# Kernel tuning notes

Measured on AMD Instinct MI355X. Metric: run time of the kernel, lower is better.

Reference implementation:

```python
import jax, jax.numpy as jnp
import numpy as np
from jax import lax

B, T, D = 1, 2048, 2048
H, KVH, HD = 16, 4, 128
BETA = 0.9
ROPE_BASE = 10000.0


def _causal_prefix_ema(x, beta):
    # x: (B, T, D); m_t = beta * m_{t-1} + (1 - beta) * x_t, m_{-1} = 0
    def step(m, xt):
        m = beta * m + (1.0 - beta) * xt
        return m, m
    _, ys = lax.scan(step, jnp.zeros_like(x[:, 0]), jnp.swapaxes(x, 0, 1))
    return jnp.swapaxes(ys, 0, 1)


def _rotate_half(x):
    x1, x2 = jnp.split(x, 2, axis=-1)
    return jnp.concatenate([-x2, x1], axis=-1)


def _rope_cos_sin(t, hd, dtype):
    inv_freq = 1.0 / (ROPE_BASE ** (jnp.arange(0, hd, 2, dtype=jnp.float32) / hd))
    freqs = jnp.arange(t, dtype=jnp.float32)[:, None] * inv_freq[None, :]  # (T, HD/2)
    emb = jnp.concatenate([freqs, freqs], axis=-1)  # (T, HD)
    return jnp.cos(emb).astype(dtype)[None, None], jnp.sin(emb).astype(dtype)[None, None]


def setup_inputs() -> dict:
    key = jax.random.key(0)
    ks = jax.random.split(key, 8)
    std = 0.02
    return {
        "hidden_states": jax.random.normal(ks[0], (B, T, D), jnp.float32),
        "Wq": jax.random.normal(ks[1], (D, H * HD), jnp.float32) * std,
        "Wk": jax.random.normal(ks[2], (D, KVH * HD), jnp.float32) * std,
        "Wv": jax.random.normal(ks[3], (D, KVH * HD), jnp.float32) * std,
        "Wo": jax.random.normal(ks[4], (H * HD, D), jnp.float32) * std,
        "Wr1": jax.random.normal(ks[5], (D, D // 2), jnp.float32) * std,
        "br1": jnp.zeros((D // 2,), jnp.float32),
        "Wr2": jax.random.normal(ks[6], (D // 2, 2), jnp.float32) * std,
        "br2": jnp.zeros((2,), jnp.float32),
    }


def reference(hidden_states, Wq, Wk, Wv, Wo, Wr1, br1, Wr2, br2):
    b, t, d = hidden_states.shape
    q = hidden_states @ Wq  # (B, T, H*HD)

    # multi-level memories: l1 = raw, l2 = causal prefix EMA
    l2 = _causal_prefix_ema(hidden_states, BETA)

    # router MLP on q + softmax over levels
    h = jax.nn.silu(q @ Wr1 + br1)
    lam = jax.nn.softmax(h @ Wr2 + br2, axis=-1)  # (B, T, 2)
    fused = lam[..., 0:1] * hidden_states + lam[..., 1:2] * l2

    # shape to heads
    q_s = q.reshape(b, t, H, HD).transpose(0, 2, 1, 3)                 # (B, H, T, HD)
    k_s = (fused @ Wk).reshape(b, t, KVH, HD).transpose(0, 2, 1, 3)    # (B, KVH, T, HD)
    v_s = (fused @ Wv).reshape(b, t, KVH, HD).transpose(0, 2, 1, 3)

    # RoPE
    cos, sin = _rope_cos_sin(t, HD, q_s.dtype)
    q_s = q_s * cos + _rotate_half(q_s) * sin
    k_s = k_s * cos + _rotate_half(k_s) * sin

    # repeat kv for GQA
    n_rep = H // KVH
    k_s = jnp.repeat(k_s, n_rep, axis=1)
    v_s = jnp.repeat(v_s, n_rep, axis=1)

    # causal SDPA
    scale = 1.0 / jnp.sqrt(jnp.asarray(HD, q_s.dtype))
    scores = jnp.einsum("bhqd,bhkd->bhqk", q_s, k_s) * scale
    causal = jnp.tril(jnp.ones((t, t), dtype=bool))
    scores = jnp.where(causal[None, None], scores, jnp.finfo(scores.dtype).min)
    attn = jax.nn.softmax(scores, axis=-1)
    out = jnp.einsum("bhqk,bhkd->bhqd", attn, v_s)  # (B, H, T, HD)

    out = out.transpose(0, 2, 1, 3).reshape(b, t, H * HD)
    return out @ Wo
```

## Files before the change

kernel.cpp:

```cpp
#include <hip/hip_runtime.h>
#include <hip/hip_bf16.h>

#define T_SEQ 2048
#define D_MODEL 2048
#define NH 16
#define NKVH 4
#define HD 128

typedef __attribute__((ext_vector_type(8))) short bf16x8;
typedef __attribute__((ext_vector_type(4))) float f32x4;

static __device__ __forceinline__ short f32_to_bf16(float f) {
    unsigned u = __float_as_uint(f);
    u += 0x7fffu + ((u >> 16) & 1u);
    return (short)(u >> 16);
}
static __device__ __forceinline__ float bf16_to_f32(short s) {
    return __uint_as_float(((unsigned)(unsigned short)s) << 16);
}
static __device__ __forceinline__ void gl_to_lds16(const void* g, void* l) {
    __builtin_amdgcn_global_load_lds(
        (const __attribute__((address_space(1))) unsigned int*)g,
        (__attribute__((address_space(3))) unsigned int*)l, 16, 0, 0);
}

template<int BN>
__global__ __launch_bounds__(256, 2) void gemm_bt_kernel(
    const short* __restrict__ A, const short* __restrict__ Bt,
    float* __restrict__ Cf, short* __restrict__ Cb,
    int M, int N, int K, const float* __restrict__ bias, int act)
{
    constexpr int NI = BN / 64;
    constexpr int BCH = BN / 32;
    __shared__ short Alds[3][64 * 64];
    __shared__ short Blds[3][BN * 64];

    const int tid = threadIdx.x;
    const int wave = tid >> 6, lane = tid & 63;
    const int l16 = lane & 15, quad = lane >> 4;
    const int wn = wave * (BN / 4);
    const int m0 = blockIdx.y * 64, n0 = blockIdx.x * BN;
    const int niter = K >> 6;

    f32x4 acc[4][NI] = {};

    #pragma unroll
    for (int st = 0; st < 2; ++st) {
        int kk0 = st << 6;
        #pragma unroll
        for (int p = 0; p < 2; ++p) {
            int li = p * 256 + tid;
            int row = li >> 3, sc = li & 7;
            gl_to_lds16(A + (size_t)(m0 + row) * K + kk0 + ((sc ^ (row & 7)) * 8),
                        &Alds[st][(size_t)(p * 256 + wave * 64) * 8]);
        }
        #pragma unroll
        for (int p = 0; p < BCH; ++p) {
            int li = p * 256 + tid;
            int row = li >> 3, sc = li & 7;
            gl_to_lds16(Bt + (size_t)(n0 + row) * K + kk0 + ((sc ^ (row & 7)) * 8),
                        &Blds[st][(size_t)(p * 256 + wave * 64) * 8]);
        }
    }

    int cur = 0, stg = 2;
    for (int t = 0; t < niter; ++t) {
        if (t + 1 < niter) {
            if constexpr (BN == 128)
                asm volatile("s_waitcnt vmcnt(6)\n\ts_barrier" ::: "memory");
            else
                asm volatile("s_waitcnt vmcnt(4)\n\ts_barrier" ::: "memory");
        } else {
            asm volatile("s_waitcnt vmcnt(0)\n\ts_barrier" ::: "memory");
        }

        if (t + 2 < niter) {
            int k1 = (t + 2) << 6;
            #pragma unroll
            for (int p = 0; p < 2; ++p) {
                int li = p * 256 + tid;
                int row = li >> 3, sc = li & 7;
                gl_to_lds16(A + (size_t)(m0 + row) * K + k1 + ((sc ^ (row & 7)) * 8),
                            &Alds[stg][(size_t)(p * 256 + wave * 64) * 8]);
            }
            #pragma unroll
            for (int p = 0; p < BCH; ++p) {
                int li = p * 256 + tid;
                int row = li >> 3, sc = li & 7;
                gl_to_lds16(Bt + (size_t)(n0 + row) * K + k1 + ((sc ^ (row & 7)) * 8),
                            &Blds[stg][(size_t)(p * 256 + wave * 64) * 8]);
            }
        }

        const short* Ab = Alds[cur];
        const short* Bb = Blds[cur];
        #pragma unroll
        for (int kk = 0; kk < 2; ++kk) {
            bf16x8 a[4], b[NI];
            #pragma unroll
            for (int i = 0; i < 4; ++i)
                a[i] = *(const bf16x8*)
                    &Ab[(size_t)(i * 16 + l16) * 64 + (((kk * 4 + quad) ^ (l16 & 7)) * 8)];
            #pragma unroll
            for (int i = 0; i < NI; ++i)
                b[i] = *(const bf16x8*)
                    &Bb[(size_t)(wn + i * 16 + l16) * 64 + (((kk * 4 + quad) ^ (l16 & 7)) * 8)];
            #pragma unroll
            for (int mi = 0; mi < 4; ++mi)
                #pragma unroll
                for (int ni = 0; ni < NI; ++ni)
                    acc[mi][ni] = __builtin_amdgcn_mfma_f32_16x16x32_bf16(
                        a[mi], b[ni], acc[mi][ni], 0, 0, 0);
        }
        cur = (cur == 2) ? 0 : cur + 1;
        stg = (stg == 2) ? 0 : stg + 1;
    }

    #pragma unroll
    for (int mi = 0; mi < 4; ++mi) {
        #pragma unroll
        for (int ni = 0; ni < NI; ++ni) {
            int col = n0 + wn + ni * 16 + l16;
            float bv = bias ? bias[col] : 0.0f;
            #pragma unroll
            for (int r = 0; r < 4; ++r) {
                int row = m0 + mi * 16 + quad * 4 + r;
                float x = acc[mi][ni][r] + bv;
                if (act) x = x / (1.0f + __expf(-x));
                size_t o = (size_t)row * N + col;
                if (Cf) Cf[o] = x;
                if (Cb) Cb[o] = f32_to_bf16(x);
            }
        }
    }
}

__global__ __launch_bounds__(256) void transpose_all_kernel(
    const float* __restrict__ Wq, const float* __restrict__ Wk,
    const float* __restrict__ Wv, const float* __restrict__ Wr1,
    const float* __restrict__ Wo, short* __restrict__ Wq_t,
    short* __restrict__ Wkv_t, short* __restrict__ Wr1_t,
    short* __restrict__ Wo_t)
{
    __shared__ float tile[32][33];
    int bx = blockIdx.x;
    const float* src; short* dst; int ld, cb;
    if (bx < 64)       { src = Wq;  dst = Wq_t;  ld = 2048; cb = bx; }
    else if (bx < 80)  { src = Wk;  dst = Wkv_t; ld = 512;  cb = bx - 64; }
    else if (bx < 96)  { src = Wv;  dst = Wkv_t + (size_t)512 * 2048; ld = 512; cb = bx - 80; }
    else if (bx < 128) { src = Wr1; dst = Wr1_t; ld = 1024; cb = bx - 96; }
    else               { src = Wo;  dst = Wo_t;  ld = 2048; cb = bx - 128; }
    int c0 = cb * 32, r0 = blockIdx.y * 32;
    int t = threadIdx.x;
    int r = t >> 3, c4 = (t & 7) * 4;
    float4 v = *(const float4*)&src[(size_t)(r0 + r) * ld + c0 + c4];
    tile[r][c4 + 0] = v.x; tile[r][c4 + 1] = v.y;
    tile[r][c4 + 2] = v.z; tile[r][c4 + 3] = v.w;
    __syncthreads();
    short o[4];
    #pragma unroll
    for (int j = 0; j < 4; ++j) o[j] = f32_to_bf16(tile[c4 + j][r]);
    *(uint2*)&dst[(size_t)(c0 + r) * 2048 + r0 + c4] = *(const uint2*)o;
}

__global__ __launch_bounds__(256) void transpose_bf_kernel(
    const short* __restrict__ src, int ld, short* __restrict__ dst, int ldd)
{
    __shared__ float tile[32][33];
    int r0 = blockIdx.y * 32, c0 = blockIdx.x * 32;
    int x = threadIdx.x & 31, y = threadIdx.x >> 5;
    #pragma unroll
    for (int i = 0; i < 4; ++i)
        tile[y + i * 8][x] = bf16_to_f32(src[(size_t)(r0 + y + i * 8) * ld + c0 + x]);
    __syncthreads();
    #pragma unroll
    for (int i = 0; i < 4; ++i)
        dst[(size_t)(c0 + y + i * 8) * ldd + r0 + x] = f32_to_bf16(tile[x][y + i * 8]);
}

__global__ __launch_bounds__(256) void ema_kernel(const float* __restrict__ hs,
                                                  float* __restrict__ l2,
                                                  short* __restrict__ hs_b)
{
    int d = blockIdx.y * 256 + threadIdx.x;
    int t0 = blockIdx.x * 128;
    int ts = t0 - 192; if (ts < 0) ts = 0;
    float m = 0.0f;
    for (int tb = ts; tb < t0; tb += 16) {
        float buf[16];
        #pragma unroll
        for (int j = 0; j < 16; ++j) buf[j] = hs[(size_t)(tb + j) * D_MODEL + d];
        #pragma unroll
        for (int j = 0; j < 16; ++j) m = 0.9f * m + 0.1f * buf[j];
    }
    for (int tb = t0; tb < t0 + 128; tb += 16) {
        float buf[16];
        #pragma unroll
        for (int j = 0; j < 16; ++j) buf[j] = hs[(size_t)(tb + j) * D_MODEL + d];
        #pragma unroll
        for (int j = 0; j < 16; ++j) hs_b[(size_t)(tb + j) * D_MODEL + d] = f32_to_bf16(buf[j]);
        #pragma unroll
        for (int j = 0; j < 16; ++j) { m = 0.9f * m + 0.1f * buf[j]; buf[j] = m; }
        #pragma unroll
        for (int j = 0; j < 16; ++j) l2[(size_t)(tb + j) * D_MODEL + d] = buf[j];
    }
}

__global__ __launch_bounds__(64) void lam_kernel(
    const short* __restrict__ h, const float* __restrict__ Wr2,
    const float* __restrict__ br2, float* __restrict__ lam)
{
    int t = blockIdx.x;
    int lane = threadIdx.x;
    float z0 = 0.0f, z1 = 0.0f;
    for (int i = lane; i < 1024; i += 64) {
        float hv = bf16_to_f32(h[(size_t)t * 1024 + i]);
        z0 += hv * Wr2[i * 2 + 0];
        z1 += hv * Wr2[i * 2 + 1];
    }
    #pragma unroll
    for (int off = 1; off < 64; off <<= 1) {
        z0 += __shfl_xor(z0, off);
        z1 += __shfl_xor(z1, off);
    }
    if (lane == 0) {
        z0 += br2[0]; z1 += br2[1];
        float mx = fmaxf(z0, z1);
        float e0 = expf(z0 - mx), e1 = expf(z1 - mx);
        float inv = 1.0f / (e0 + e1);
        lam[t * 2 + 0] = e0 * inv;
        lam[t * 2 + 1] = e1 * inv;
    }
}

__global__ void fuse_kernel(const float* __restrict__ hs, const float* __restrict__ l2,
                            const float* __restrict__ lam, short* __restrict__ fused)
{
    int idx = blockIdx.x * blockDim.x + threadIdx.x;
    int t = idx >> 9;
    float a0 = lam[t * 2 + 0], a1 = lam[t * 2 + 1];
    float4 a = ((const float4*)hs)[idx];
    float4 b = ((const float4*)l2)[idx];
    short o[4] = {f32_to_bf16(a0 * a.x + a1 * b.x), f32_to_bf16(a0 * a.y + a1 * b.y),
                  f32_to_bf16(a0 * a.z + a1 * b.z), f32_to_bf16(a0 * a.w + a1 * b.w)};
    *(uint2*)(fused + (size_t)idx * 4) = *(const uint2*)o;
}

__global__ void rope_q_kernel(const short* __restrict__ q, short* __restrict__ qr)
{
    int idx = blockIdx.x * blockDim.x + threadIdx.x;
    int d = idx & 63;
    int h = (idx >> 6) & 15;
    int t = idx >> 10;
    float fr = (float)t * __expf(-(float)d * 0.14391156831212787f);
    float s, c;
    sincosf(fr, &s, &c);
    const float sc = 0.08838834764831845f;
    const short* src = q + (size_t)t * D_MODEL + h * HD;
    float x1 = bf16_to_f32(src[d]) * sc, x2 = bf16_to_f32(src[d + 64]) * sc;
    short* dst = qr + ((size_t)h * T_SEQ + t) * HD;
    dst[d]      = f32_to_bf16(x1 * c - x2 * s);
    dst[d + 64] = f32_to_bf16(x2 * c + x1 * s);
}

__global__ void rope_k_kernel(const short* __restrict__ kv, short* __restrict__ kr)
{
    int idx = blockIdx.x * blockDim.x + threadIdx.x;
    int d = idx & 63;
    int kh = (idx >> 6) & 3;
    int t = idx >> 8;
    float fr = (float)t * __expf(-(float)d * 0.14391156831212787f);
    float s, c;
    sincosf(fr, &s, &c);
    const short* src = kv + (size_t)t * 1024 + kh * HD;
    float x1 = bf16_to_f32(src[d]), x2 = bf16_to_f32(src[d + 64]);
    short* dst = kr + ((size_t)kh * T_SEQ + t) * HD;
    dst[d]      = f32_to_bf16(x1 * c - x2 * s);
    dst[d + 64] = f32_to_bf16(x2 * c + x1 * s);
}

__global__ __launch_bounds__(512, 2) void attn_kernel(
    const short* __restrict__ Qr, const short* __restrict__ Kr,
    const short* __restrict__ Vt, short* __restrict__ Out)
{
    const int h = blockIdx.x;
    const int y = blockIdx.y;
    const int kvh = h >> 2;
    const int tid = threadIdx.x;
    const int wave = tid >> 6, lane = tid & 63;
    const int l16 = lane & 15, quad = lane >> 4;
    const int wq = wave & 1;
    const int wk = wave >> 1;

    __shared__ __align__(16) char smem[147456];
    short* Klds = (short*)smem;
    short* Vlds = (short*)(smem + 65536);
    short* Plds = (short*)(smem + 131072);

    const short* kbase = Kr + (size_t)kvh * T_SEQ * HD;
    const short* vbase = Vt + (size_t)kvh * HD * T_SEQ;

    #pragma unroll 1
    for (int ph = 0; ph < 2; ++ph) {
        const int qt32 = ph ? (31 - y) : y;
        const int qbase = qt32 * 64 + wq * 32;
        const int n = (qt32 >> 1) + 1;
        const int ko = wk * 32;

        bf16x8 qf[2][4];
        #pragma unroll
        for (int m = 0; m < 2; ++m) {
            const short* qrow = Qr + ((size_t)h * T_SEQ + qbase + m * 16 + l16) * HD;
            #pragma unroll
            for (int kc = 0; kc < 4; ++kc)
                qf[m][kc] = *(const bf16x8*)&qrow[kc * 32 + quad * 8];
        }
        f32x4 o[2][8] = {};
        float lsum[2][4] = {};

        __syncthreads();

        {
            #pragma unroll
            for (int p = 0; p < 4; ++p) {
                int li = p * 512 + tid;
                int row = li >> 4, gs = (li & 15) ^ (row & 15);
                gl_to_lds16(kbase + (size_t)row * HD + gs * 8,
                            &Klds[(size_t)(p * 512 + wave * 64) * 8]);
            }
            #pragma unroll
            for (int p = 0; p < 4; ++p) {
                int li = p * 512 + tid;
                int row = li >> 4, gs = (li & 15) ^ (row & 15);
                gl_to_lds16(vbase + (size_t)row * T_SEQ + gs * 8,
                            &Vlds[(size_t)(p * 512 + wave * 64) * 8]);
            }
        }

        for (int t = 0; t < n; ++t) {
            asm volatile("s_waitcnt vmcnt(0)\n\ts_barrier" ::: "memory");

            if (t + 1 < n) {
                int kv1 = (t + 1) << 7;
                int nb = (t + 1) & 1;
                const short* ks = kbase + (size_t)kv1 * HD;
                #pragma unroll
                for (int p = 0; p < 4; ++p) {
                    int li = p * 512 + tid;
                    int row = li >> 4, gs = (li & 15) ^ (row & 15);
                    gl_to_lds16(ks + (size_t)row * HD + gs * 8,
                                &Klds[(size_t)(nb * 16384 + (p * 512 + wave * 64) * 8)]);
                }
                #pragma unroll
                for (int p = 0; p < 4; ++p) {
                    int li = p * 512 + tid;
                    int row = li >> 4, gs = (li & 15) ^ (row & 15);
                    gl_to_lds16(vbase + (size_t)row * T_SEQ + kv1 + gs * 8,
                                &Vlds[(size_t)(nb * 16384 + (p * 512 + wave * 64) * 8)]);
                }
            }

            const short* Kb = Klds + (size_t)(t & 1) * 16384;
            const short* Vb = Vlds + (size_t)(t & 1) * 16384;

            f32x4 s[2][2];
            #pragma unroll
            for (int m = 0; m < 2; ++m)
                #pragma unroll
                for (int ni = 0; ni < 2; ++ni) s[m][ni] = (f32x4){0, 0, 0, 0};
            __builtin_amdgcn_s_setprio(1);
            #pragma unroll
            for (int ni = 0; ni < 2; ++ni)
                #pragma unroll
                for (int kc = 0; kc < 4; ++kc) {
                    bf16x8 b = *(const bf16x8*)
                        &Kb[(size_t)(ko + ni * 16 + l16) * 128 + (((kc * 4 + quad) ^ l16) * 8)];
                    s[0][ni] = __builtin_amdgcn_mfma_f32_16x16x32_bf16(qf[0][kc], b, s[0][ni], 0, 0, 0);
                    s[1][ni] = __builtin_amdgcn_mfma_f32_16x16x32_bf16(qf[1][kc], b, s[1][ni], 0, 0, 0);
                }
            __builtin_amdgcn_s_setprio(0);

            if (t == n - 1) {
                int kvg0 = (t << 7) + ko;
                #pragma unroll
                for (int m = 0; m < 2; ++m)
                    #pragma unroll
                    for (int ni = 0; ni < 2; ++ni) {
                        int kvg = kvg0 + ni * 16 + l16;
                        #pragma unroll
                        for (int r = 0; r < 4; ++r) {
                            int qg = qbase + m * 16 + quad * 4 + r;
                            float p = (kvg <= qg) ? __expf(s[m][ni][r]) : 0.0f;
                            lsum[m][r] += p;
                            int prow = quad * 4 + r, pcol = ni * 16 + l16;
                            int slot = (pcol >> 3) ^ (prow & 3) ^ quad;
                            Plds[wave * 1024 + (m * 16 + prow) * 32 +
                                 slot * 8 + (pcol & 7)] = f32_to_bf16(p);
                        }
                    }
            } else {
                #pragma unroll
                for (int m = 0; m < 2; ++m)
                    #pragma unroll
                    for (int ni = 0; ni < 2; ++ni)
                        #pragma unroll
                        for (int r = 0; r < 4; ++r) {
                            float p = __expf(s[m][ni][r]);
                            lsum[m][r] += p;
                            int prow = quad * 4 + r, pcol = ni * 16 + l16;
                            int slot = (pcol >> 3) ^ (prow & 3) ^ quad;
                            Plds[wave * 1024 + (m * 16 + prow) * 32 +
                                 slot * 8 + (pcol & 7)] = f32_to_bf16(p);
                        }
            }
            asm volatile("s_waitcnt lgkmcnt(0)" ::: "memory");

            __builtin_amdgcn_s_setprio(1);
            {
                int slot0 = quad ^ (l16 & 3) ^ ((l16 >> 2) & 3);
                bf16x8 pa0 = *(const bf16x8*)
                    &Plds[wave * 1024 + l16 * 32 + slot0 * 8];
                bf16x8 pa1 = *(const bf16x8*)
                    &Plds[wave * 1024 + (16 + l16) * 32 + slot0 * 8];
                #pragma unroll
                for (int d8 = 0; d8 < 8; ++d8) {
                    bf16x8 b = *(const bf16x8*)
                        &Vb[(size_t)(d8 * 16 + l16) * 128 +
                            (((wk * 4 + quad) ^ l16) * 8)];
                    o[0][d8] = __builtin_amdgcn_mfma_f32_16x16x32_bf16(pa0, b, o[0][d8], 0, 0, 0);
                    o[1][d8] = __builtin_amdgcn_mfma_f32_16x16x32_bf16(pa1, b, o[1][d8], 0, 0, 0);
                }
            }
            __builtin_amdgcn_s_setprio(0);
        }

        __syncthreads();
        float* Ox = (float*)smem;
        float* Lx = (float*)(smem + 101376);
        if (wk) {
            int base = (wq * 3 + wk - 1) * 32;
            #pragma unroll
            for (int m = 0; m < 2; ++m)
                #pragma unroll
                for (int d8 = 0; d8 < 8; ++d8)
                    #pragma unroll
                    for (int r = 0; r < 4; ++r)
                        Ox[(base + m * 16 + quad * 4 + r) * 132 + d8 * 16 + l16] = o[m][d8][r];
            #pragma unroll
            for (int m = 0; m < 2; ++m)
                #pragma unroll
                for (int r = 0; r < 4; ++r)
                    Lx[(base + m * 16 + quad * 4 + r) * 16 + l16] = lsum[m][r];
        }
        __syncthreads();
        if (wk == 0) {
            #pragma unroll
            for (int j = 0; j < 3; ++j)
                #pragma unroll
                for (int m = 0; m < 2; ++m)
                    #pragma unroll
                    for (int d8 = 0; d8 < 8; ++d8)
                        #pragma unroll
                        for (int r = 0; r < 4; ++r)
                            o[m][d8][r] += Ox[((wq * 3 + j) * 32 + m * 16 + quad * 4 + r) * 132
                                              + d8 * 16 + l16];
            #pragma unroll
            for (int m = 0; m < 2; ++m)
                #pragma unroll
                for (int r = 0; r < 4; ++r) {
                    #pragma unroll
                    for (int j = 0; j < 3; ++j)
                        lsum[m][r] += Lx[((wq * 3 + j) * 32 + m * 16 + quad * 4 + r) * 16 + l16];
                    #pragma unroll
                    for (int off = 1; off < 16; off <<= 1)
                        lsum[m][r] += __shfl_xor(lsum[m][r], off);
                    lsum[m][r] = 1.0f / lsum[m][r];
                }
            #pragma unroll
            for (int m = 0; m < 2; ++m)
                #pragma unroll
                for (int d8 = 0; d8 < 8; ++d8)
                    #pragma unroll
                    for (int r = 0; r < 4; ++r) {
                        int row = qbase + m * 16 + quad * 4 + r;
                        Out[(size_t)row * D_MODEL + h * HD + d8 * 16 + l16] =
                            f32_to_bf16(o[m][d8][r] * lsum[m][r]);
                    }
        }
    }
}

extern "C" void kernel_launch(void* const* d_in, const int* in_sizes, int n_in,
                              void* d_out, int out_size, void* d_ws, size_t ws_size,
                              hipStream_t stream)
{
    const float* hs  = (const float*)d_in[0];
    const float* Wq  = (const float*)d_in[1];
    const float* Wk  = (const float*)d_in[2];
    const float* Wv  = (const float*)d_in[3];
    const float* Wo  = (const float*)d_in[4];
    const float* Wr1 = (const float*)d_in[5];
    const float* br1 = (const float*)d_in[6];
    const float* Wr2 = (const float*)d_in[7];
    const float* br2 = (const float*)d_in[8];
    float* out = (float*)d_out;

    char* w = (char*)d_ws;
    const size_t MB = 1u << 20;
    float* l2_f     = (float*)(w + 0 * MB);
    short* hs_bf    = (short*)(w + 16 * MB);
    short* Wq_t     = (short*)(w + 24 * MB);
    short* Wkv_t    = (short*)(w + 32 * MB);
    short* Wr1_t    = (short*)(w + 36 * MB);
    short* Wo_t     = (short*)(w + 40 * MB);
    short* q_bf     = (short*)(w + 48 * MB);
    short* h_bf     = (short*)(w + 56 * MB);
    short* fused_bf = (short*)(w + 60 * MB);
    short* kv_bf    = (short*)(w + 68 * MB);
    short* qr       = (short*)(w + 72 * MB);
    short* kr       = (short*)(w + 80 * MB);
    short* vr       = (short*)(w + 82 * MB);
    float* lam_f    = (float*)(w + 84 * MB);
    short* attn_bf  = hs_bf;

    transpose_all_kernel<<<dim3(192, 64), 256, 0, stream>>>(
        Wq, Wk, Wv, Wr1, Wo, Wq_t, Wkv_t, Wr1_t, Wo_t);

    ema_kernel<<<dim3(T_SEQ / 128, D_MODEL / 256), 256, 0, stream>>>(hs, l2_f, hs_bf);

    gemm_bt_kernel<128><<<dim3(16, 32), 256, 0, stream>>>(
        hs_bf, Wq_t, nullptr, q_bf, 2048, 2048, 2048, nullptr, 0);

    gemm_bt_kernel<64><<<dim3(16, 32), 256, 0, stream>>>(
        q_bf, Wr1_t, nullptr, h_bf, 2048, 1024, 2048, br1, 1);

    lam_kernel<<<T_SEQ, 64, 0, stream>>>(h_bf, Wr2, br2, lam_f);

    fuse_kernel<<<(T_SEQ * D_MODEL / 4) / 256, 256, 0, stream>>>(hs, l2_f, lam_f, fused_bf);

    gemm_bt_kernel<64><<<dim3(16, 32), 256, 0, stream>>>(
        fused_bf, Wkv_t, nullptr, kv_bf, 2048, 1024, 2048, nullptr, 0);

    rope_q_kernel<<<(T_SEQ * NH * 64) / 256, 256, 0, stream>>>(q_bf, qr);
    rope_k_kernel<<<(T_SEQ * NKVH * 64) / 256, 256, 0, stream>>>(kv_bf, kr);
    transpose_bf_kernel<<<dim3(16, 64), 256, 0, stream>>>(kv_bf + 512, 1024, vr, 2048);

    attn_kernel<<<dim3(NH, 16), 512, 0, stream>>>(qr, kr, vr, attn_bf);

    gemm_bt_kernel<128><<<dim3(16, 32), 256, 0, stream>>>(
        attn_bf, Wo_t, out, nullptr, 2048, 2048, 2048, nullptr, 0);
}
```

Before: 313.4 us.

## Load K/V fragments directly from global into registers, drop LDS staging

The attention kernel no longer double-buffers K and V tiles in LDS with async global-to-LDS copies and per-tile barriers. Each wave now loads its own K and V MFMA fragments straight from global memory into registers and keeps only a small padded per-wave P buffer in LDS, replacing the XOR swizzle with a row stride of 40. This removes block-wide barriers and LDS traffic and shrinks shared memory use. In exchange, global/L2 traffic rises because the waves sharing a KV tile each fetch it themselves, and the load latency is exposed with no prefetch.

```diff
diff --git a/kernel.cpp b/kernel.cpp
--- a/kernel.cpp
+++ b/kernel.cpp
@@ -292,20 +292,21 @@
     const int wq = wave & 1;
     const int wk = wave >> 1;
 
-    __shared__ __align__(16) char smem[147456];
-    short* Klds = (short*)smem;
-    short* Vlds = (short*)(smem + 65536);
-    short* Plds = (short*)(smem + 131072);
+    __shared__ __align__(16) char smem[113664];
+    short* Plds = (short*)smem;
 
     const short* kbase = Kr + (size_t)kvh * T_SEQ * HD;
     const short* vbase = Vt + (size_t)kvh * HD * T_SEQ;
+
+    const int ko = wk * 32;
+    const short* kfrag = kbase + (size_t)(ko + l16) * HD + quad * 8;
+    const short* vfrag = vbase + (size_t)l16 * T_SEQ + ko + quad * 8;
 
     #pragma unroll 1
     for (int ph = 0; ph < 2; ++ph) {
         const int qt32 = ph ? (31 - y) : y;
         const int qbase = qt32 * 64 + wq * 32;
         const int n = (qt32 >> 1) + 1;
-        const int ko = wk * 32;
 
         bf16x8 qf[2][4];
         #pragma unroll
@@ -320,48 +321,16 @@
 
         __syncthreads();
 
-        {
-            #pragma unroll
-            for (int p = 0; p < 4; ++p) {
-                int li = p * 512 + tid;
-                int row = li >> 4, gs = (li & 15) ^ (row & 15);
-                gl_to_lds16(kbase + (size_t)row * HD + gs * 8,
-                            &Klds[(size_t)(p * 512 + wave * 64) * 8]);
-            }
-            #pragma unroll
-            for (int p = 0; p < 4; ++p) {
-                int li = p * 512 + tid;
-                int row = li >> 4, gs = (li & 15) ^ (row & 15);
-                gl_to_lds16(vbase + (size_t)row * T_SEQ + gs * 8,
-                            &Vlds[(size_t)(p * 512 + wave * 64) * 8]);
-            }
-        }
-
         for (int t = 0; t < n; ++t) {
-            asm volatile("s_waitcnt vmcnt(0)\n\ts_barrier" ::: "memory");
-
-            if (t + 1 < n) {
-                int kv1 = (t + 1) << 7;
-                int nb = (t + 1) & 1;
-                const short* ks = kbase + (size_t)kv1 * HD;
-                #pragma unroll
-                for (int p = 0; p < 4; ++p) {
-                    int li = p * 512 + tid;
-                    int row = li >> 4, gs = (li & 15) ^ (row & 15);
-                    gl_to_lds16(ks + (size_t)row * HD + gs * 8,
-                                &Klds[(size_t)(nb * 16384 + (p * 512 + wave * 64) * 8)]);
-                }
-                #pragma unroll
-                for (int p = 0; p < 4; ++p) {
-                    int li = p * 512 + tid;
-                    int row = li >> 4, gs = (li & 15) ^ (row & 15);
-                    gl_to_lds16(vbase + (size_t)row * T_SEQ + kv1 + gs * 8,
-                                &Vlds[(size_t)(nb * 16384 + (p * 512 + wave * 64) * 8)]);
-                }
-            }
-
-            const short* Kb = Klds + (size_t)(t & 1) * 16384;
-            const short* Vb = Vlds + (size_t)(t & 1) * 16384;
+            const int kvt = t << 7;
+
+            bf16x8 kb[2][4];
+            #pragma unroll
+            for (int ni = 0; ni < 2; ++ni)
+                #pragma unroll
+                for (int kc = 0; kc < 4; ++kc)
+                    kb[ni][kc] = *(const bf16x8*)
+                        &kfrag[(size_t)(kvt + ni * 16) * HD + kc * 32];
 
             f32x4 s[2][2];
             #pragma unroll
@@ -373,15 +342,22 @@
             for (int ni = 0; ni < 2; ++ni)
                 #pragma unroll
                 for (int kc = 0; kc < 4; ++kc) {
-                    bf16x8 b = *(const bf16x8*)
-                        &Kb[(size_t)(ko + ni * 16 + l16) * 128 + (((kc * 4 + quad) ^ l16) * 8)];
-                    s[0][ni] = __builtin_amdgcn_mfma_f32_16x16x32_bf16(qf[0][kc], b, s[0][ni], 0, 0, 0);
-                    s[1][ni] = __builtin_amdgcn_mfma_f32_16x16x32_bf16(qf[1][kc], b, s[1][ni], 0, 0, 0);
+                    s[0][ni] = __builtin_amdgcn_mfma_f32_16x16x32_bf16(
+                        qf[0][kc], kb[ni][kc], s[0][ni], 0, 0, 0);
+                    s[1][ni] = __builtin_amdgcn_mfma_f32_16x16x32_bf16(
+                        qf[1][kc], kb[ni][kc], s[1][ni], 0, 0, 0);
                 }
             __builtin_amdgcn_s_setprio(0);
 
+            bf16x8 vb[8];
+            #pragma unroll
+            for (int d8 = 0; d8 < 8; ++d8)
+                vb[d8] = *(const bf16x8*)
+                    &vfrag[(size_t)(d8 * 16) * T_SEQ + kvt];
+
+            short* Pw = Plds + wave * 1280;
             if (t == n - 1) {
-                int kvg0 = (t << 7) + ko;
+                int kvg0 = kvt + ko;
                 #pragma unroll
                 for (int m = 0; m < 2; ++m)
                     #pragma unroll
@@ -392,10 +368,8 @@
                             int qg = qbase + m * 16 + quad * 4 + r;
                             float p = (kvg <= qg) ? __expf(s[m][ni][r]) : 0.0f;
                             lsum[m][r] += p;
-                            int prow = quad * 4 + r, pcol = ni * 16 + l16;
-                            int slot = (pcol >> 3) ^ (prow & 3) ^ quad;
-                            Plds[wave * 1024 + (m * 16 + prow) * 32 +
-                                 slot * 8 + (pcol & 7)] = f32_to_bf16(p);
+                            Pw[(m * 16 + quad * 4 + r) * 40 + ni * 16 + l16] =
+                                f32_to_bf16(p);
                         }
                     }
             } else {
@@ -407,28 +381,22 @@
                         for (int r = 0; r < 4; ++r) {
                             float p = __expf(s[m][ni][r]);
                             lsum[m][r] += p;
-                            int prow = quad * 4 + r, pcol = ni * 16 + l16;
-                            int slot = (pcol >> 3) ^ (prow & 3) ^ quad;
-                            Plds[wave * 1024 + (m * 16 + prow) * 32 +
-                                 slot * 8 + (pcol & 7)] = f32_to_bf16(p);
+                            Pw[(m * 16 + quad * 4 + r) * 40 + ni * 16 + l16] =
+                                f32_to_bf16(p);
                         }
             }
             asm volatile("s_waitcnt lgkmcnt(0)" ::: "memory");
 
             __builtin_amdgcn_s_setprio(1);
             {
-                int slot0 = quad ^ (l16 & 3) ^ ((l16 >> 2) & 3);
-                bf16x8 pa0 = *(const bf16x8*)
-                    &Plds[wave * 1024 + l16 * 32 + slot0 * 8];
-                bf16x8 pa1 = *(const bf16x8*)
-                    &Plds[wave * 1024 + (16 + l16) * 32 + slot0 * 8];
+                bf16x8 pa0 = *(const bf16x8*)&Pw[l16 * 40 + quad * 8];
+                bf16x8 pa1 = *(const bf16x8*)&Pw[(16 + l16) * 40 + quad * 8];
                 #pragma unroll
                 for (int d8 = 0; d8 < 8; ++d8) {
-                    bf16x8 b = *(const bf16x8*)
-                        &Vb[(size_t)(d8 * 16 + l16) * 128 +
-                            (((wk * 4 + quad) ^ l16) * 8)];
-                    o[0][d8] = __builtin_amdgcn_mfma_f32_16x16x32_bf16(pa0, b, o[0][d8], 0, 0, 0);
-                    o[1][d8] = __builtin_amdgcn_mfma_f32_16x16x32_bf16(pa1, b, o[1][d8], 0, 0, 0);
+                    o[0][d8] = __builtin_amdgcn_mfma_f32_16x16x32_bf16(
+                        pa0, vb[d8], o[0][d8], 0, 0, 0);
+                    o[1][d8] = __builtin_amdgcn_mfma_f32_16x16x32_bf16(
+                        pa1, vb[d8], o[1][d8], 0, 0, 0);
                 }
             }
             __builtin_amdgcn_s_setprio(0);
```

After: 350.1 us. +11.7%, slower.
